# Kernel tuning notes

Measured on AMD Instinct MI355X. Metric: run time of the kernel, lower is better.

## Reference

```python
import jax, jax.numpy as jnp
import numpy as np
from jax import lax

D_MODEL, D_INNER, D_CONV, DT_RANK, D_STATE, SEQ_LEN = 1024, 2048, 4, 64, 16, 4096


def setup_inputs() -> dict:
    key = jax.random.key(0)
    ks = jax.random.split(key, 9)
    s = 0.02
    x = jax.random.normal(ks[0], (SEQ_LEN, D_MODEL), dtype=jnp.float32)
    W_in = jax.random.normal(ks[1], (2 * D_INNER, D_MODEL), dtype=jnp.float32) * s
    conv_w = jax.random.normal(ks[2], (D_INNER, 1, D_CONV), dtype=jnp.float32) * 0.2  # depthwise (O,I/g,K)
    conv_b = jax.random.normal(ks[3], (D_INNER,), dtype=jnp.float32) * s
    W_x = jax.random.normal(ks[4], (DT_RANK + 2 * D_STATE, D_INNER), dtype=jnp.float32) * s
    W_dt = jax.random.normal(ks[5], (D_INNER, DT_RANK), dtype=jnp.float32) * s
    b_dt = jax.random.normal(ks[6], (D_INNER,), dtype=jnp.float32) * s
    # canonical S4D-real init: A[d, n] = n+1 -> A_log = log(1..d_state), tiled over d_inner
    A_log = jnp.log(jnp.tile(jnp.arange(1, D_STATE + 1, dtype=jnp.float32), (D_INNER, 1)))
    D = jnp.ones((D_INNER,), dtype=jnp.float32)
    W_out = jax.random.normal(ks[7], (D_MODEL, D_INNER), dtype=jnp.float32) * s
    return {"x": x, "W_in": W_in, "conv_w": conv_w, "conv_b": conv_b,
            "W_x": W_x, "W_dt": W_dt, "b_dt": b_dt, "A_log": A_log, "D": D,
            "W_out": W_out}


def _causal_depthwise_conv(x_ld, conv_w, conv_b):
    # x_ld: (L, d_inner). eqx Conv1d with padding=d_conv-1 then [:, :L] == left-pad causal conv.
    k = conv_w.shape[-1]
    xp = jnp.pad(x_ld, ((k - 1, 0), (0, 0)))  # (L+k-1, d)
    lhs = xp.T[None]  # (1, d, L+k-1)
    out = lax.conv_general_dilated(
        lhs, conv_w, window_strides=(1,), padding='VALID',
        dimension_numbers=('NCH', 'OIH', 'NCH'),
        feature_group_count=x_ld.shape[1])  # (1, d, L)
    return (out[0] + conv_b[:, None]).T  # (L, d)


def reference(x, W_in, conv_w, conv_b, W_x, W_dt, b_dt, A_log, D, W_out):
    L = x.shape[0]
    d_inner, d_state = A_log.shape
    dt_rank = W_dt.shape[1]

    xr = x @ W_in.T                      # (L, 2*d_inner)
    xi, res = jnp.split(xr, 2, axis=-1)  # each (L, d_inner)
    xs = jax.nn.silu(_causal_depthwise_conv(xi, conv_w, conv_b))  # (L, d_inner)

    # selective SSM
    dbl = xs @ W_x.T                     # (L, dt_rank + 2*d_state)
    dt_in, B, C = jnp.split(dbl, [dt_rank, dt_rank + d_state], axis=-1)
    delta = jax.nn.softplus(dt_in @ W_dt.T + b_dt)       # (L, d_inner)
    A = -jnp.exp(A_log)                                  # (d_inner, d_state)
    dA = jnp.exp(delta[:, :, None] * A[None])            # (L, d, n)
    dBu = delta[:, :, None] * B[:, None, :] * xs[:, :, None]  # (L, d, n)

    def step(h, ab):
        a, b = ab
        h = a * h + b
        return h, h

    _, hs = lax.scan(step, jnp.zeros((d_inner, d_state), dtype=x.dtype), (dA, dBu))
    y = jnp.einsum('ldn,ln->ld', hs, C) + xs * D         # (L, d_inner)

    y = y * jax.nn.silu(res)
    return y @ W_out.T                                   # (L, d_model)
```

## Files before the change

### kernel.cpp

```cpp
#include <hip/hip_runtime.h>
#include <cstdint>
#include <cstddef>

#define LSEQ 4096
#define DM 1024
#define DI 2048
#define DCONV 4
#define DRNK 64
#define DSTATE 16
#define DXW 96
#define NCH 64
#define CLEN 64
#define KSPLIT 16

typedef unsigned short ushort_t;
typedef __bf16 bfx8 __attribute__((ext_vector_type(8)));
typedef float  fx4  __attribute__((ext_vector_type(4)));
typedef ushort_t usx8 __attribute__((ext_vector_type(8)));

__device__ __forceinline__ float siluf(float x) { return x / (1.f + __expf(-x)); }
__device__ __forceinline__ float softplusf(float x) {
  return fmaxf(x, 0.f) + log1pf(__expf(-fabsf(x)));
}
__device__ __forceinline__ ushort_t f2b(float x) {
  __bf16 b = (__bf16)x;
  return __builtin_bit_cast(ushort_t, b);
}
__device__ __forceinline__ float b2f(ushort_t u) {
  unsigned int x = ((unsigned int)u) << 16;
  return __builtin_bit_cast(float, x);
}
__device__ __forceinline__ void async16(const void* g, void* l) {
  __builtin_amdgcn_global_load_lds(
      (const __attribute__((address_space(1))) unsigned int*)g,
      (__attribute__((address_space(3))) unsigned int*)l, 16, 0, 0);
}

template <int EPI, int BN>
__global__ __launch_bounds__(256) void gemm_bf16(
    const ushort_t* __restrict__ A, int lda,
    const ushort_t* __restrict__ B, int ldb,
    void* __restrict__ Cv, int ldc, int K,
    const float* __restrict__ bias)
{
  constexpr int NJ = BN / 32;
  __shared__ ushort_t As[128 * 32];
  __shared__ ushort_t Bs[BN * 32];
  const int tid  = threadIdx.x;
  const int m0   = blockIdx.y * 128, n0 = blockIdx.x * BN;
  const int lane = tid & 63;
  const int wave = tid >> 6;
  const int wm   = (wave >> 1) * 64, wn = (wave & 1) * (BN / 2);
  const int lm   = lane & 15;
  const int r0 = tid >> 2;
  const int cswz = (((tid & 3) ^ ((r0 >> 1) & 3))) * 8;
  const int swz = (((lane >> 4) ^ ((lm >> 1) & 3))) * 8;

  fx4 acc[4][NJ] = {};

  const ushort_t* ga = A + (size_t)(m0 + r0) * lda + cswz;
  const ushort_t* gb = B + (size_t)(n0 + r0) * ldb + cswz;
  ushort_t* la0 = &As[r0 * 32 + (tid & 3) * 8];
  ushort_t* la1 = &As[(r0 + 64) * 32 + (tid & 3) * 8];
  ushort_t* lb0 = &Bs[r0 * 32 + (tid & 3) * 8];
  ushort_t* lb1 = (BN == 128) ? &Bs[(r0 + 64) * 32 + (tid & 3) * 8] : nullptr;

  for (int k0 = 0; k0 < K; k0 += 32) {
    async16(ga + k0, la0);
    async16(ga + (size_t)64 * lda + k0, la1);
    async16(gb + k0, lb0);
    if (BN == 128) async16(gb + (size_t)64 * ldb + k0, lb1);
    __syncthreads();

    bfx8 af[4], bfr[NJ];
#pragma unroll
    for (int i = 0; i < 4; ++i)
      af[i] = *(const bfx8*)&As[(wm + i * 16 + lm) * 32 + swz];
#pragma unroll
    for (int j = 0; j < NJ; ++j)
      bfr[j] = *(const bfx8*)&Bs[(wn + j * 16 + lm) * 32 + swz];
#pragma unroll
    for (int i = 0; i < 4; ++i)
#pragma unroll
      for (int j = 0; j < NJ; ++j)
        acc[i][j] = __builtin_amdgcn_mfma_f32_16x16x32_bf16(af[i], bfr[j], acc[i][j], 0, 0, 0);
    __syncthreads();
  }

  const int crow = (lane >> 4) * 4;
  const int ccol = lane & 15;
#pragma unroll
  for (int i = 0; i < 4; ++i)
#pragma unroll
    for (int r = 0; r < 4; ++r) {
      const size_t rowoff = (size_t)(m0 + wm + i * 16 + crow + r) * ldc + n0 + wn + ccol;
      if (EPI == 1) {
        ushort_t* cp = (ushort_t*)Cv + rowoff;
#pragma unroll
        for (int j = 0; j < NJ; ++j) cp[j * 16] = f2b(acc[i][j][r]);
      } else if (EPI == 2) {
        ushort_t* cp = (ushort_t*)Cv + rowoff;
        const int nb = n0 + wn + ccol;
#pragma unroll
        for (int j = 0; j < NJ; ++j)
          cp[j * 16] = f2b(softplusf(acc[i][j][r] + bias[nb + j * 16]));
      } else {
        float* cp = (float*)Cv + rowoff;
#pragma unroll
        for (int j = 0; j < NJ; ++j) cp[j * 16] = acc[i][j][r];
      }
    }
}

__global__ __launch_bounds__(256) void gemm_dbl(
    const ushort_t* __restrict__ A, const ushort_t* __restrict__ B,
    float* __restrict__ P)
{
  __shared__ ushort_t As[128 * 32];
  __shared__ ushort_t Bs[128 * 32];
  const int tid  = threadIdx.x;
  const int m0   = blockIdx.y * 128;
  const int lane = tid & 63;
  const int wave = tid >> 6;
  const int wm   = (wave >> 1) * 64, wn = (wave & 1) * 48;
  const int lm   = lane & 15;
  const int r0 = tid >> 2;
  const int cswz = (((tid & 3) ^ ((r0 >> 1) & 3))) * 8;
  const int swz  = (((lane >> 4) ^ ((lm >> 1) & 3))) * 8;
  const int kbeg = blockIdx.z * (DI / KSPLIT);

  fx4 acc[4][3] = {};

  const int brow1 = (r0 + 64 < DXW) ? r0 + 64 : DXW - 1;
  const ushort_t* ga  = A + (size_t)(m0 + r0) * DI + kbeg + cswz;
  const ushort_t* gb0 = B + (size_t)r0 * DI + kbeg + cswz;
  const ushort_t* gb1 = B + (size_t)brow1 * DI + kbeg + cswz;
  ushort_t* la0 = &As[r0 * 32 + (tid & 3) * 8];
  ushort_t* la1 = &As[(r0 + 64) * 32 + (tid & 3) * 8];
  ushort_t* lb0 = &Bs[r0 * 32 + (tid & 3) * 8];
  ushort_t* lb1 = &Bs[(r0 + 64) * 32 + (tid & 3) * 8];

  for (int k0 = 0; k0 < DI / KSPLIT; k0 += 32) {
    async16(ga + k0, la0);
    async16(ga + (size_t)64 * DI + k0, la1);
    async16(gb0 + k0, lb0);
    async16(gb1 + k0, lb1);
    __syncthreads();

    bfx8 af[4], bfr[3];
#pragma unroll
    for (int i = 0; i < 4; ++i)
      af[i] = *(const bfx8*)&As[(wm + i * 16 + lm) * 32 + swz];
#pragma unroll
    for (int j = 0; j < 3; ++j)
      bfr[j] = *(const bfx8*)&Bs[(wn + j * 16 + lm) * 32 + swz];
#pragma unroll
    for (int i = 0; i < 4; ++i)
#pragma unroll
      for (int j = 0; j < 3; ++j)
        acc[i][j] = __builtin_amdgcn_mfma_f32_16x16x32_bf16(af[i], bfr[j], acc[i][j], 0, 0, 0);
    __syncthreads();
  }

  float* base = P + (size_t)blockIdx.z * LSEQ * DXW;
  const int crow = (lane >> 4) * 4;
  const int ccol = lane & 15;
#pragma unroll
  for (int i = 0; i < 4; ++i)
#pragma unroll
    for (int r = 0; r < 4; ++r) {
      float* cp = base + (size_t)(m0 + wm + i * 16 + crow + r) * DXW + wn + ccol;
#pragma unroll
      for (int j = 0; j < 3; ++j)
        cp[j * 16] = acc[i][j][r];
    }
}

__global__ __launch_bounds__(256) void reduce_dbl(
    const float* __restrict__ P, ushort_t* __restrict__ dtb,
    float* __restrict__ dblBC)
{
  const int f = blockIdx.x * 256 + threadIdx.x;
  float s = 0.f;
#pragma unroll
  for (int z = 0; z < KSPLIT; ++z) s += P[(size_t)z * LSEQ * DXW + f];
  const int l = f / DXW;
  const int c = f - l * DXW;
  if (c < DRNK) dtb[(size_t)l * DRNK + c] = f2b(s);
  else          dblBC[(size_t)l * 32 + (c - DRNK)] = s;
}

#define CSZ0 (LSEQ * DM)
#define CSZ1 (2 * DI * DM)
#define CSZ2 (DM * DI)
#define CSZ3 (DXW * DI)
#define CSZ4 (DI * DRNK)
#define CTOT (CSZ0 + CSZ1 + CSZ2 + CSZ3 + CSZ4)

__global__ __launch_bounds__(256) void cast_all(
    const float* __restrict__ x, const float* __restrict__ W_in,
    const float* __restrict__ W_out, const float* __restrict__ W_x,
    const float* __restrict__ W_dt,
    ushort_t* __restrict__ xb, ushort_t* __restrict__ W_inb,
    ushort_t* __restrict__ W_outb, ushort_t* __restrict__ W_xb,
    ushort_t* __restrict__ W_dtb)
{
  int i = (blockIdx.x * 256 + threadIdx.x) * 4;
  if (i >= CTOT) return;
  const float* src; ushort_t* dst;
  if (i < CSZ0) { src = x + i; dst = xb + i; }
  else if (i < CSZ0 + CSZ1) { int o = i - CSZ0; src = W_in + o; dst = W_inb + o; }
  else if (i < CSZ0 + CSZ1 + CSZ2) { int o = i - CSZ0 - CSZ1; src = W_out + o; dst = W_outb + o; }
  else if (i < CSZ0 + CSZ1 + CSZ2 + CSZ3) { int o = i - CSZ0 - CSZ1 - CSZ2; src = W_x + o; dst = W_xb + o; }
  else { int o = i - CSZ0 - CSZ1 - CSZ2 - CSZ3; src = W_dt + o; dst = W_dtb + o; }
  float4 v = *(const float4*)src;
  ushort4 o4;
  o4.x = f2b(v.x); o4.y = f2b(v.y); o4.z = f2b(v.z); o4.w = f2b(v.w);
  *(ushort4*)dst = o4;
}

__global__ __launch_bounds__(256) void conv2(
    const ushort_t* __restrict__ xrb, const float* __restrict__ cw,
    const float* __restrict__ cb, ushort_t* __restrict__ xsb)
{
  const int d0 = threadIdx.x * 8;
  const int l0 = blockIdx.x * 8;

  float4 w[8];
#pragma unroll
  for (int j = 0; j < 8; ++j) w[j] = *(const float4*)(cw + (size_t)(d0 + j) * DCONV);
  float cbv[8];
  *(float4*)&cbv[0] = *(const float4*)(cb + d0);
  *(float4*)&cbv[4] = *(const float4*)(cb + d0 + 4);

  float h0[8], h1[8], h2[8];
#pragma unroll
  for (int j = 0; j < 8; ++j) { h0[j] = 0.f; h1[j] = 0.f; h2[j] = 0.f; }
  if (l0 >= 3) {
    usx8 u0 = *(const usx8*)(xrb + (size_t)(l0 - 3) * (2 * DI) + d0);
    usx8 u1 = *(const usx8*)(xrb + (size_t)(l0 - 2) * (2 * DI) + d0);
    usx8 u2 = *(const usx8*)(xrb + (size_t)(l0 - 1) * (2 * DI) + d0);
#pragma unroll
    for (int j = 0; j < 8; ++j) { h0[j] = b2f(u0[j]); h1[j] = b2f(u1[j]); h2[j] = b2f(u2[j]); }
  }

#pragma unroll
  for (int i = 0; i < 8; ++i) {
    const int l = l0 + i;
    usx8 uc = *(const usx8*)(xrb + (size_t)l * (2 * DI) + d0);
    float c[8];
#pragma unroll
    for (int j = 0; j < 8; ++j) c[j] = b2f(uc[j]);
    usx8 o;
#pragma unroll
    for (int j = 0; j < 8; ++j) {
      float acc = cbv[j];
      acc = fmaf(w[j].x, h0[j], acc);
      acc = fmaf(w[j].y, h1[j], acc);
      acc = fmaf(w[j].z, h2[j], acc);
      acc = fmaf(w[j].w, c[j], acc);
      o[j] = f2b(siluf(acc));
    }
    *(usx8*)(xsb + (size_t)l * DI + d0) = o;
#pragma unroll
    for (int j = 0; j < 8; ++j) { h0[j] = h1[j]; h1[j] = h2[j]; h2[j] = c[j]; }
  }
}

__global__ __launch_bounds__(256) void scan_pass1(
    const ushort_t* __restrict__ deltab, const ushort_t* __restrict__ xsb,
    const float* __restrict__ dblBC, const float* __restrict__ A_log,
    float* __restrict__ cP, float* __restrict__ cS)
{
  const int tid = threadIdx.x;
  const int g = blockIdx.x;
  const int c = blockIdx.y;
  const int d = g * 256 + tid;
  __shared__ ushort_t Dsh[CLEN * 256];
  __shared__ ushort_t Ush[CLEN * 256];
  __shared__ float Bsh[CLEN][DSTATE];

  const size_t rowbase = (size_t)(c * CLEN) * DI + g * 256;
  for (int i = tid; i < CLEN * 32; i += 256) {
    const int l = i >> 5;
    const int o = (i & 31) * 8;
    *(usx8*)&Dsh[l * 256 + o] = *(const usx8*)(deltab + rowbase + (size_t)l * DI + o);
    *(usx8*)&Ush[l * 256 + o] = *(const usx8*)(xsb   + rowbase + (size_t)l * DI + o);
  }
  for (int i = tid; i < CLEN * DSTATE; i += 256) {
    const int l = i >> 4, n = i & 15;
    Bsh[l][n] = dblBC[(size_t)(c * CLEN + l) * 32 + n];
  }
  __syncthreads();

  float Av[DSTATE], h[DSTATE], P[DSTATE];
#pragma unroll
  for (int n = 0; n < DSTATE; ++n) {
    Av[n] = -__expf(A_log[d * DSTATE + n]);
    h[n] = 0.f; P[n] = 1.f;
  }
  for (int l = 0; l < CLEN; ++l) {
    const float dlt = b2f(Dsh[l * 256 + tid]);
    const float du = dlt * b2f(Ush[l * 256 + tid]);
#pragma unroll
    for (int n = 0; n < DSTATE; ++n) {
      const float dA = __expf(dlt * Av[n]);
      h[n] = fmaf(dA, h[n], du * Bsh[l][n]);
      P[n] *= dA;
    }
  }
  const size_t base = (size_t)c * DI * DSTATE + (size_t)d * DSTATE;
#pragma unroll
  for (int n = 0; n < DSTATE; ++n) { cP[base + n] = P[n]; cS[base + n] = h[n]; }
}

__global__ __launch_bounds__(256) void scan_pass2(
    const float* __restrict__ cP, const float* __restrict__ cS,
    float* __restrict__ ch0)
{
  const int dn = blockIdx.x * 256 + threadIdx.x;
  float h = 0.f;
  for (int c = 0; c < NCH; ++c) {
    const size_t o = (size_t)c * DI * DSTATE + dn;
    const float p = cP[o], s = cS[o];
    ch0[o] = h;
    h = fmaf(p, h, s);
  }
}

__global__ __launch_bounds__(256) void scan_pass3(
    const ushort_t* __restrict__ deltab, const ushort_t* __restrict__ xsb,
    const float* __restrict__ dblBC, const float* __restrict__ A_log,
    const float* __restrict__ ch0, const float* __restrict__ Dp,
    const ushort_t* __restrict__ xrb, ushort_t* __restrict__ y1b)
{
  const int tid = threadIdx.x;
  const int g = blockIdx.x;
  const int c = blockIdx.y;
  const int d = g * 256 + tid;
  __shared__ ushort_t Dsh[CLEN * 256];
  __shared__ ushort_t Ush[CLEN * 256];
  __shared__ float Bsh[CLEN][DSTATE];
  __shared__ float Csh[CLEN][DSTATE];

  const size_t rowbase = (size_t)(c * CLEN) * DI + g * 256;
  for (int i = tid; i < CLEN * 32; i += 256) {
    const int l = i >> 5;
    const int o = (i & 31) * 8;
    *(usx8*)&Dsh[l * 256 + o] = *(const usx8*)(deltab + rowbase + (size_t)l * DI + o);
    *(usx8*)&Ush[l * 256 + o] = *(const usx8*)(xsb   + rowbase + (size_t)l * DI + o);
  }
  for (int i = tid; i < CLEN * DSTATE; i += 256) {
    const int l = i >> 4, n = i & 15;
    const size_t row = (size_t)(c * CLEN + l) * 32;
    Bsh[l][n] = dblBC[row + n];
    Csh[l][n] = dblBC[row + 16 + n];
  }
  __syncthreads();

  float Av[DSTATE], h[DSTATE];
  const size_t base = (size_t)c * DI * DSTATE + (size_t)d * DSTATE;
#pragma unroll
  for (int n = 0; n < DSTATE; ++n) {
    Av[n] = -__expf(A_log[d * DSTATE + n]);
    h[n] = ch0[base + n];
  }
  const float Dd = Dp[d];
  const ushort_t* resp = xrb + (size_t)(c * CLEN) * (2 * DI) + DI + d;
  ushort_t* yp = y1b + (size_t)(c * CLEN) * DI + d;
  for (int l = 0; l < CLEN; ++l) {
    const float dlt = b2f(Dsh[l * 256 + tid]);
    const float u = b2f(Ush[l * 256 + tid]);
    const float du = dlt * u;
    float y = 0.f;
#pragma unroll
    for (int n = 0; n < DSTATE; ++n) {
      const float dA = __expf(dlt * Av[n]);
      h[n] = fmaf(dA, h[n], du * Bsh[l][n]);
      y = fmaf(h[n], Csh[l][n], y);
    }
    y = fmaf(u, Dd, y);
    const float res = b2f(resp[(size_t)l * (2 * DI)]);
    yp[(size_t)l * DI] = f2b(y * siluf(res));
  }
}

extern "C" void kernel_launch(void* const* d_in, const int* in_sizes, int n_in,
                              void* d_out, int out_size, void* d_ws, size_t ws_size,
                              hipStream_t stream) {
  (void)in_sizes; (void)n_in; (void)out_size; (void)ws_size;
  const float* x      = (const float*)d_in[0];
  const float* W_in   = (const float*)d_in[1];
  const float* conv_w = (const float*)d_in[2];
  const float* conv_b = (const float*)d_in[3];
  const float* W_x    = (const float*)d_in[4];
  const float* W_dt   = (const float*)d_in[5];
  const float* b_dt   = (const float*)d_in[6];
  const float* A_log  = (const float*)d_in[7];
  const float* Dp     = (const float*)d_in[8];
  const float* W_out  = (const float*)d_in[9];
  float* out = (float*)d_out;

  float* ws    = (float*)d_ws;
  float* cP    = ws;
  float* cS    = cP + (size_t)NCH * DI * DSTATE;
  ushort_t* deltab = (ushort_t*)(cS + (size_t)NCH * DI * DSTATE);
  ushort_t* xrb   = deltab + (size_t)LSEQ * DI;
  ushort_t* xsb   = xrb   + (size_t)LSEQ * 2 * DI;
  ushort_t* y1b   = xsb   + (size_t)LSEQ * DI;
  ushort_t* xb    = y1b   + (size_t)LSEQ * DI;
  ushort_t* W_inb = xb    + (size_t)LSEQ * DM;
  ushort_t* W_outb= W_inb + (size_t)2 * DI * DM;
  ushort_t* W_xb  = W_outb+ (size_t)DM * DI;
  ushort_t* W_dtb = W_xb  + (size_t)DXW * DI;
  ushort_t* dtb   = W_dtb + (size_t)DI * DRNK;
  float* dblBC = (float*)(dtb + (size_t)LSEQ * DRNK);
  float* partial = cP;
  float* ch0 = cP;

  hipLaunchKernelGGL(cast_all, dim3((CTOT / 4 + 255) / 256), dim3(256), 0, stream,
                     x, W_in, W_out, W_x, W_dt, xb, W_inb, W_outb, W_xb, W_dtb);

  hipLaunchKernelGGL(HIP_KERNEL_NAME(gemm_bf16<1, 128>),
                     dim3((2 * DI) / 128, LSEQ / 128), dim3(256), 0, stream,
                     xb, DM, W_inb, DM, (void*)xrb, 2 * DI, DM, nullptr);

  hipLaunchKernelGGL(conv2, dim3(LSEQ / 8), dim3(256), 0, stream,
                     xrb, conv_w, conv_b, xsb);

  hipLaunchKernelGGL(gemm_dbl, dim3(1, LSEQ / 128, KSPLIT), dim3(256), 0, stream,
                     xsb, W_xb, partial);
  hipLaunchKernelGGL(reduce_dbl, dim3((LSEQ * DXW) / 256), dim3(256), 0, stream,
                     partial, dtb, dblBC);

  hipLaunchKernelGGL(HIP_KERNEL_NAME(gemm_bf16<2, 128>),
                     dim3(DI / 128, LSEQ / 128), dim3(256), 0, stream,
                     dtb, DRNK, W_dtb, DRNK, (void*)deltab, DI, DRNK, b_dt);

  hipLaunchKernelGGL(scan_pass1, dim3(DI / 256, NCH), dim3(256), 0, stream,
                     deltab, xsb, dblBC, A_log, cP, cS);
  hipLaunchKernelGGL(scan_pass2, dim3((DI * DSTATE) / 256), dim3(256), 0, stream,
                     cP, cS, ch0);
  hipLaunchKernelGGL(scan_pass3, dim3(DI / 256, NCH), dim3(256), 0, stream,
                     deltab, xsb, dblBC, A_log, ch0, Dp, xrb, y1b);

  hipLaunchKernelGGL(HIP_KERNEL_NAME(gemm_bf16<0, 64>),
                     dim3(DM / 64, LSEQ / 128), dim3(256), 0, stream,
                     y1b, DI, W_outb, DI, (void*)out, DM, DI, nullptr);
}
```

Before: 330.9 us.

## Fuse three scan passes into one cooperative kernel with grid syncs

Replaces the three-kernel chunked scan (chunk summaries, cross-chunk prefix, final pass) with a single cooperative kernel that keeps delta, xs and B/C tiles in shared memory across all phases and separates the phases with grid-wide barriers. This avoids reloading the delta and xs tiles from global memory in the final pass and removes two kernel launches. It also halves the K-split of the dbl GEMM. The cooperative launch needs all 512 blocks of 256 threads with about 66KB of shared memory each to be resident at once, and grid syncs add barrier latency. The serial prefix phase now runs on only a subset of blocks while the rest wait.

```diff
diff --git a/kernel.cpp b/kernel.cpp
--- a/kernel.cpp
+++ b/kernel.cpp
@@ -1,6 +1,9 @@
 #include <hip/hip_runtime.h>
+#include <hip/hip_cooperative_groups.h>
 #include <cstdint>
 #include <cstddef>
+
+namespace cg = cooperative_groups;
 
 #define LSEQ 4096
 #define DM 1024
@@ -11,7 +14,7 @@
 #define DXW 96
 #define NCH 64
 #define CLEN 64
-#define KSPLIT 16
+#define KSPLIT 8
 
 typedef unsigned short ushort_t;
 typedef __bf16 bfx8 __attribute__((ext_vector_type(8)));
@@ -267,73 +270,14 @@
   }
 }
 
-__global__ __launch_bounds__(256) void scan_pass1(
+__global__ __launch_bounds__(256) void scan_fused(
     const ushort_t* __restrict__ deltab, const ushort_t* __restrict__ xsb,
     const float* __restrict__ dblBC, const float* __restrict__ A_log,
-    float* __restrict__ cP, float* __restrict__ cS)
-{
-  const int tid = threadIdx.x;
-  const int g = blockIdx.x;
-  const int c = blockIdx.y;
-  const int d = g * 256 + tid;
-  __shared__ ushort_t Dsh[CLEN * 256];
-  __shared__ ushort_t Ush[CLEN * 256];
-  __shared__ float Bsh[CLEN][DSTATE];
-
-  const size_t rowbase = (size_t)(c * CLEN) * DI + g * 256;
-  for (int i = tid; i < CLEN * 32; i += 256) {
-    const int l = i >> 5;
-    const int o = (i & 31) * 8;
-    *(usx8*)&Dsh[l * 256 + o] = *(const usx8*)(deltab + rowbase + (size_t)l * DI + o);
-    *(usx8*)&Ush[l * 256 + o] = *(const usx8*)(xsb   + rowbase + (size_t)l * DI + o);
-  }
-  for (int i = tid; i < CLEN * DSTATE; i += 256) {
-    const int l = i >> 4, n = i & 15;
-    Bsh[l][n] = dblBC[(size_t)(c * CLEN + l) * 32 + n];
-  }
-  __syncthreads();
-
-  float Av[DSTATE], h[DSTATE], P[DSTATE];
-#pragma unroll
-  for (int n = 0; n < DSTATE; ++n) {
-    Av[n] = -__expf(A_log[d * DSTATE + n]);
-    h[n] = 0.f; P[n] = 1.f;
-  }
-  for (int l = 0; l < CLEN; ++l) {
-    const float dlt = b2f(Dsh[l * 256 + tid]);
-    const float du = dlt * b2f(Ush[l * 256 + tid]);
-#pragma unroll
-    for (int n = 0; n < DSTATE; ++n) {
-      const float dA = __expf(dlt * Av[n]);
-      h[n] = fmaf(dA, h[n], du * Bsh[l][n]);
-      P[n] *= dA;
-    }
-  }
-  const size_t base = (size_t)c * DI * DSTATE + (size_t)d * DSTATE;
-#pragma unroll
-  for (int n = 0; n < DSTATE; ++n) { cP[base + n] = P[n]; cS[base + n] = h[n]; }
-}
-
-__global__ __launch_bounds__(256) void scan_pass2(
-    const float* __restrict__ cP, const float* __restrict__ cS,
-    float* __restrict__ ch0)
-{
-  const int dn = blockIdx.x * 256 + threadIdx.x;
-  float h = 0.f;
-  for (int c = 0; c < NCH; ++c) {
-    const size_t o = (size_t)c * DI * DSTATE + dn;
-    const float p = cP[o], s = cS[o];
-    ch0[o] = h;
-    h = fmaf(p, h, s);
-  }
-}
-
-__global__ __launch_bounds__(256) void scan_pass3(
-    const ushort_t* __restrict__ deltab, const ushort_t* __restrict__ xsb,
-    const float* __restrict__ dblBC, const float* __restrict__ A_log,
-    const float* __restrict__ ch0, const float* __restrict__ Dp,
-    const ushort_t* __restrict__ xrb, ushort_t* __restrict__ y1b)
-{
+    const float* __restrict__ Dp, const ushort_t* __restrict__ xrb,
+    ushort_t* __restrict__ y1b,
+    float* __restrict__ cP, float* __restrict__ cS, float* __restrict__ ch0)
+{
+  cg::grid_group gg = cg::this_grid();
   const int tid = threadIdx.x;
   const int g = blockIdx.x;
   const int c = blockIdx.y;
@@ -358,13 +302,44 @@
   }
   __syncthreads();
 
-  float Av[DSTATE], h[DSTATE];
-  const size_t base = (size_t)c * DI * DSTATE + (size_t)d * DSTATE;
+  float Av[DSTATE], h[DSTATE], P[DSTATE];
 #pragma unroll
   for (int n = 0; n < DSTATE; ++n) {
     Av[n] = -__expf(A_log[d * DSTATE + n]);
-    h[n] = ch0[base + n];
-  }
+    h[n] = 0.f; P[n] = 1.f;
+  }
+  for (int l = 0; l < CLEN; ++l) {
+    const float dlt = b2f(Dsh[l * 256 + tid]);
+    const float du = dlt * b2f(Ush[l * 256 + tid]);
+#pragma unroll
+    for (int n = 0; n < DSTATE; ++n) {
+      const float dA = __expf(dlt * Av[n]);
+      h[n] = fmaf(dA, h[n], du * Bsh[l][n]);
+      P[n] *= dA;
+    }
+  }
+  const size_t base = (size_t)c * DI * DSTATE + (size_t)d * DSTATE;
+#pragma unroll
+  for (int n = 0; n < DSTATE; ++n) { cP[base + n] = P[n]; cS[base + n] = h[n]; }
+
+  gg.sync();
+
+  const int bid = blockIdx.y * gridDim.x + blockIdx.x;
+  if (bid < (DI * DSTATE) / 256) {
+    const int dn = bid * 256 + tid;
+    float hh = 0.f;
+    for (int cc = 0; cc < NCH; ++cc) {
+      const size_t o = (size_t)cc * DI * DSTATE + dn;
+      const float p = cP[o], s = cS[o];
+      ch0[o] = hh;
+      hh = fmaf(p, hh, s);
+    }
+  }
+
+  gg.sync();
+
+#pragma unroll
+  for (int n = 0; n < DSTATE; ++n) h[n] = ch0[base + n];
   const float Dd = Dp[d];
   const ushort_t* resp = xrb + (size_t)(c * CLEN) * (2 * DI) + DI + d;
   ushort_t* yp = y1b + (size_t)(c * CLEN) * DI + d;
@@ -437,12 +412,14 @@
                      dim3(DI / 128, LSEQ / 128), dim3(256), 0, stream,
                      dtb, DRNK, W_dtb, DRNK, (void*)deltab, DI, DRNK, b_dt);
 
-  hipLaunchKernelGGL(scan_pass1, dim3(DI / 256, NCH), dim3(256), 0, stream,
-                     deltab, xsb, dblBC, A_log, cP, cS);
-  hipLaunchKernelGGL(scan_pass2, dim3((DI * DSTATE) / 256), dim3(256), 0, stream,
-                     cP, cS, ch0);
-  hipLaunchKernelGGL(scan_pass3, dim3(DI / 256, NCH), dim3(256), 0, stream,
-                     deltab, xsb, dblBC, A_log, ch0, Dp, xrb, y1b);
+  {
+    void* args[] = { (void*)&deltab, (void*)&xsb, (void*)&dblBC, (void*)&A_log,
+                     (void*)&Dp, (void*)&xrb, (void*)&y1b,
+                     (void*)&cP, (void*)&cS, (void*)&ch0 };
+    hipLaunchCooperativeKernel((void*)scan_fused,
+                               dim3(DI / 256, NCH), dim3(256),
+                               args, 0, stream);
+  }
 
   hipLaunchKernelGGL(HIP_KERNEL_NAME(gemm_bf16<0, 64>),
                      dim3(DM / 64, LSEQ / 128), dim3(256), 0, stream,
```

Measured after the change: 464.1 us. 1.4x slower.
